# Optimization experiments

Hardware: AMD Instinct MI355X
Metric: run time of the kernel (lower is better)

## Reference

```python
import jax, jax.numpy as jnp
import numpy as np

K = 16

def _knn_idx(pts, k):
    # pts: [B, 3, N] -> idx [B, N, k] (self-inclusive nearest neighbors)
    inner = -2.0 * jnp.einsum('bdn,bdm->bnm', pts, pts)
    xx = jnp.sum(pts * pts, axis=1)  # [B, N]
    pd = -xx[:, :, None] - inner - xx[:, None, :]  # negative squared distance
    _, idx = jax.lax.top_k(pd, k)
    return idx

def _gather(feats, idx):
    # feats: [B, N, D], idx: [B, N, k] -> [B, N, k, D]
    return jax.vmap(lambda f, i: f[i])(feats, idx)

def _conv1x1(x, w, b):
    # x: [B, Cin, N], w: [Cout, Cin], b: [Cout]
    return jnp.einsum('oi,bin->bon', w, x) + b[None, :, None]

def _linear(x, w, b):
    # x: [B, N, Din], w: [Dout, Din]
    return jnp.einsum('bnd,od->bno', x, w) + b

def _local_cov(pts, idx):
    # pts: [B, 3, N] -> [B, 12, N]
    nb = _gather(jnp.swapaxes(pts, 1, 2), idx)  # [B, N, k, 3]
    outer = nb[:, :, 0, :, None] * nb[:, :, 1, None, :]  # [B, N, 3, 3]
    B, N = pts.shape[0], pts.shape[2]
    outer = jnp.swapaxes(outer.reshape(B, N, 9), 1, 2)  # [B, 9, N]
    return jnp.concatenate([pts, outer], axis=1)

def _local_maxpool(x, idx):
    # x: [B, D, N] -> [B, N, D]
    nb = _gather(jnp.swapaxes(x, 1, 2), idx)  # [B, N, k, D]
    return jnp.max(nb, axis=2)

def setup_inputs() -> dict:
    key = jax.random.key(0)
    ks = jax.random.split(key, 20)
    def w(k, shape):
        return jax.random.normal(k, shape, dtype=jnp.float32) * 0.05
    pts = jax.random.normal(ks[0], (8, 3, 4096), dtype=jnp.float32)
    return {
        'pts': pts,
        'm1w1': w(ks[1], (64, 12)), 'm1b1': w(ks[2], (64,)),
        'm1w2': w(ks[3], (64, 64)), 'm1b2': w(ks[4], (64,)),
        'm1w3': w(ks[5], (64, 64)), 'm1b3': w(ks[6], (64,)),
        'l1w': w(ks[7], (64, 64)), 'l1b': w(ks[8], (64,)),
        'c1w': w(ks[9], (128, 64)), 'c1b': w(ks[10], (128,)),
        'l2w': w(ks[11], (128, 128)), 'l2b': w(ks[12], (128,)),
        'c2w': w(ks[13], (1024, 128)), 'c2b': w(ks[14], (1024,)),
        'm2w1': w(ks[15], (512, 1024)), 'm2b1': w(ks[16], (512,)),
        'm2w2': w(ks[17], (512, 512)), 'm2b2': w(ks[18], (512,)),
    }

def reference(pts, m1w1, m1b1, m1w2, m1b2, m1w3, m1b3, l1w, l1b,
              c1w, c1b, l2w, l2b, c2w, c2b, m2w1, m2b1, m2w2, m2b2):
    idx = _knn_idx(pts, K)  # [B, N, k]
    x = _local_cov(pts, idx)  # [B, 12, N]
    # mlp1: three 1x1 convs with ReLU
    x = jax.nn.relu(_conv1x1(x, m1w1, m1b1))
    x = jax.nn.relu(_conv1x1(x, m1w2, m1b2))
    x = jax.nn.relu(_conv1x1(x, m1w3, m1b3))  # [B, 64, N]
    # graph layer
    x = _local_maxpool(x, idx)          # [B, N, 64]
    x = _linear(x, l1w, l1b)            # [B, N, 64]
    x = jnp.swapaxes(x, 1, 2)           # [B, 64, N]
    x = jax.nn.relu(_conv1x1(x, c1w, c1b))  # [B, 128, N]
    x = _local_maxpool(x, idx)          # [B, N, 128]
    x = _linear(x, l2w, l2b)            # [B, N, 128]
    x = jnp.swapaxes(x, 1, 2)           # [B, 128, N]
    x = _conv1x1(x, c2w, c2b)           # [B, 1024, N]
    # global max pool
    x = jnp.max(x, axis=2, keepdims=True)  # [B, 1024, 1]
    # mlp2
    x = jax.nn.relu(_conv1x1(x, m2w1, m2b1))
    x = _conv1x1(x, m2w2, m2b2)  # [B, 512, 1]
    return x.reshape(-1, 512)
```

## Files before the change

### kernel.cpp

```cpp
#include <hip/hip_runtime.h>
#include <cfloat>

#define NBATCH 8
#define NPTS   4096
#define KNN    16
#define PPB    32
#define NSL    8
#define CAP    24

__device__ __forceinline__ float relu_f(float x) { return x > 0.f ? x : 0.f; }

__global__ __launch_bounds__(256)
void knn_kernel(const float* __restrict__ pts, int* __restrict__ idxout)
{
    __shared__ __align__(16) float4 tile[NSL * 129];
    __shared__ float  kl[PPB * NSL * 8];
    __shared__ float  thr[PPB];
    __shared__ int    cnt[PPB];

    const int b = blockIdx.y, tid = threadIdx.x;
    const int ptl = tid >> 3, r = tid & 7;
    const int n = blockIdx.x * PPB + ptl;
    const float* pb = pts + (size_t)b * 3 * NPTS;

    const float sx = pb[n], sy = pb[NPTS + n], sz = pb[2 * NPTS + n];

    float k8[8];
#pragma unroll
    for (int s = 0; s < 8; ++s) k8[s] = -FLT_MAX;

    const float4* slice = tile + r * 129;

    for (int t = 0; t < 4; ++t) {
        if (t) __syncthreads();
        for (int i = tid; i < 1024; i += 256) {
            int j = t * 1024 + i;
            float x = pb[j], y = pb[NPTS + j], z = pb[2 * NPTS + j];
            float xx = __fadd_rn(__fadd_rn(__fmul_rn(x, x), __fmul_rn(y, y)),
                                 __fmul_rn(z, z));
            tile[(i >> 7) * 129 + (i & 127)] = make_float4(x, y, z, xx);
        }
        __syncthreads();
#pragma unroll 8
        for (int ii = 0; ii < 128; ++ii) {
            float4 c = slice[ii];
            float dt = __fmaf_rn(sx, c.x, __fmaf_rn(sy, c.y, __fmul_rn(sz, c.z)));
            float pd = __fmaf_rn(2.f, dt, -c.w);
            float old0 = k8[0];
#pragma unroll
            for (int s = 7; s >= 1; --s)
                k8[s] = __builtin_amdgcn_fmed3f(k8[s - 1], k8[s], pd);
            k8[0] = fmaxf(old0, pd);
        }
    }

#pragma unroll
    for (int s = 0; s < 8; ++s) kl[(ptl * NSL + r) * 8 + s] = k8[s];
    __syncthreads();

    if (r == 0) {
        const float* L = kl + ptl * 64;
        int p0 = 0, p1 = 0, p2 = 0, p3 = 0, p4 = 0, p5 = 0, p6 = 0, p7 = 0;
        float tv = 0.f;
        for (int o = 0; o < 16; ++o) {
            float v0 = (p0 < 8) ? L[p0]      : -FLT_MAX;
            float v1 = (p1 < 8) ? L[8 + p1]  : -FLT_MAX;
            float v2 = (p2 < 8) ? L[16 + p2] : -FLT_MAX;
            float v3 = (p3 < 8) ? L[24 + p3] : -FLT_MAX;
            float v4 = (p4 < 8) ? L[32 + p4] : -FLT_MAX;
            float v5 = (p5 < 8) ? L[40 + p5] : -FLT_MAX;
            float v6 = (p6 < 8) ? L[48 + p6] : -FLT_MAX;
            float v7 = (p7 < 8) ? L[56 + p7] : -FLT_MAX;
            float m = fmaxf(fmaxf(fmaxf(v0, v1), fmaxf(v2, v3)),
                            fmaxf(fmaxf(v4, v5), fmaxf(v6, v7)));
            tv = m;
            if      (v0 == m) ++p0;
            else if (v1 == m) ++p1;
            else if (v2 == m) ++p2;
            else if (v3 == m) ++p3;
            else if (v4 == m) ++p4;
            else if (v5 == m) ++p5;
            else if (v6 == m) ++p6;
            else              ++p7;
        }
        thr[ptl] = tv;
        cnt[ptl] = 0;
    }
    __syncthreads();
    const float myThr = thr[ptl];

    float* pv = kl;
    int*   pi = (int*)(kl + PPB * CAP);

    for (int tt = 0; tt < 4; ++tt) {
        int t = 3 - tt;
        if (tt) {
            __syncthreads();
            for (int i = tid; i < 1024; i += 256) {
                int j = t * 1024 + i;
                float x = pb[j], y = pb[NPTS + j], z = pb[2 * NPTS + j];
                float xx = __fadd_rn(__fadd_rn(__fmul_rn(x, x), __fmul_rn(y, y)),
                                     __fmul_rn(z, z));
                tile[(i >> 7) * 129 + (i & 127)] = make_float4(x, y, z, xx);
            }
            __syncthreads();
        }
#pragma unroll 8
        for (int ii = 0; ii < 128; ++ii) {
            float4 c = slice[ii];
            float dt = __fmaf_rn(sx, c.x, __fmaf_rn(sy, c.y, __fmul_rn(sz, c.z)));
            float pd = __fmaf_rn(2.f, dt, -c.w);
            if (pd >= myThr) {
                int pos = atomicAdd(&cnt[ptl], 1);
                if (pos < CAP) {
                    pv[ptl * CAP + pos] = pd;
                    pi[ptl * CAP + pos] = t * 1024 + r * 128 + ii;
                }
            }
        }
    }
    __syncthreads();

    if (tid < PPB) {
        const int np = blockIdx.x * PPB + tid;
        int* out = idxout + ((size_t)b * NPTS + np) * KNN;
        int c = cnt[tid];
        if (c <= CAP) {
            float* v  = pv + tid * CAP;
            int*   ix = pi + tid * CAP;
            for (int o = 0; o < 16; ++o) {
                int best = o;
                for (int q = o + 1; q < c; ++q) {
                    float vq = v[q], vb = v[best];
                    if (vq > vb || (vq == vb && ix[q] < ix[best])) best = q;
                }
                float tv = v[o]; v[o] = v[best]; v[best] = tv;
                int   ti = ix[o]; ix[o] = ix[best]; ix[best] = ti;
                out[o] = ix[o];
            }
        } else {
            float qx = pb[np], qy = pb[NPTS + np], qz = pb[2 * NPTS + np];
            float v16[16]; int i16[16];
#pragma unroll
            for (int s = 0; s < 16; ++s) { v16[s] = -FLT_MAX; i16[s] = 0; }
            for (int j = 0; j < NPTS; ++j) {
                float x = pb[j], y = pb[NPTS + j], z = pb[2 * NPTS + j];
                float xx = __fadd_rn(__fadd_rn(__fmul_rn(x, x), __fmul_rn(y, y)),
                                     __fmul_rn(z, z));
                float dt = __fmaf_rn(qx, x, __fmaf_rn(qy, y, __fmul_rn(qz, z)));
                float pd = __fmaf_rn(2.f, dt, -xx);
                if (pd > v16[15]) {
                    int s = 15;
                    while (s > 0 && pd > v16[s - 1]) {
                        v16[s] = v16[s - 1]; i16[s] = i16[s - 1]; --s;
                    }
                    v16[s] = pd; i16[s] = j;
                }
            }
            for (int o = 0; o < 16; ++o) out[o] = i16[o];
        }
    }
}

__global__ __launch_bounds__(256)
void cov_mlp1_kernel(const float* __restrict__ pts, const int* __restrict__ idx,
                     const float* __restrict__ w1, const float* __restrict__ b1,
                     const float* __restrict__ w2, const float* __restrict__ b2,
                     const float* __restrict__ w3, const float* __restrict__ b3,
                     float* __restrict__ h3out)
{
    __shared__ __align__(16) float cov[64 * 16];
    __shared__ __align__(16) float w1s[64 * 16];
    __shared__ __align__(16) float w2s[64 * 68];
    __shared__ __align__(16) float w3s[64 * 68];
    __shared__ __align__(16) float hA[64 * 68];
    __shared__ __align__(16) float hB[64 * 68];

    const int b = blockIdx.y, tid = threadIdx.x;
    const int n0 = blockIdx.x * 64;
    const int pq = tid >> 4, cq = tid & 15;

    for (int i = tid; i < 64 * 4; i += 256) {
        int p = i >> 2, k4 = i & 3;
        float4 v = make_float4(0.f, 0.f, 0.f, 0.f);
        if (k4 < 3) v = *(const float4*)(w1 + p * 12 + k4 * 4);
        ((float4*)(w1s + p * 16))[k4] = v;
    }
    for (int i = tid; i < 64 * 16; i += 256) {
        int p = i >> 4, k4 = i & 15;
        ((float4*)(w2s + p * 68))[k4] = ((const float4*)(w2 + p * 64))[k4];
        ((float4*)(w3s + p * 68))[k4] = ((const float4*)(w3 + p * 64))[k4];
    }
    if (tid < 64) {
        const int n = n0 + tid;
        const int* ip = idx + ((size_t)b * NPTS + n) * KNN;
        int j0 = ip[0], j1 = ip[1];
        const float* pb = pts + (size_t)b * 3 * NPTS;
        float px = pb[n],  py = pb[NPTS + n],  pz = pb[2 * NPTS + n];
        float ax = pb[j0], ay = pb[NPTS + j0], az = pb[2 * NPTS + j0];
        float bx = pb[j1], by = pb[NPTS + j1], bz = pb[2 * NPTS + j1];
        float* cv = cov + tid * 16;
        cv[0] = px; cv[1] = py; cv[2] = pz;
        cv[3] = ax * bx; cv[4]  = ax * by; cv[5]  = ax * bz;
        cv[6] = ay * bx; cv[7]  = ay * by; cv[8]  = ay * bz;
        cv[9] = az * bx; cv[10] = az * by; cv[11] = az * bz;
        cv[12] = 0.f; cv[13] = 0.f; cv[14] = 0.f; cv[15] = 0.f;
    }
    __syncthreads();

    {
        float acc[4][4];
#pragma unroll
        for (int i = 0; i < 4; ++i)
#pragma unroll
            for (int j = 0; j < 4; ++j) acc[i][j] = 0.f;
        const float4* X4 = (const float4*)cov;
        const float4* W4 = (const float4*)w1s;
#pragma unroll
        for (int k4 = 0; k4 < 4; ++k4) {
            float4 xa[4], wb[4];
#pragma unroll
            for (int i = 0; i < 4; ++i) xa[i] = X4[(pq * 4 + i) * 4 + k4];
#pragma unroll
            for (int j = 0; j < 4; ++j) wb[j] = W4[(cq + 16 * j) * 4 + k4];
#pragma unroll
            for (int i = 0; i < 4; ++i)
#pragma unroll
                for (int j = 0; j < 4; ++j)
                    acc[i][j] += xa[i].x * wb[j].x + xa[i].y * wb[j].y
                               + xa[i].z * wb[j].z + xa[i].w * wb[j].w;
        }
#pragma unroll
        for (int j = 0; j < 4; ++j) {
            int c = cq + 16 * j;
            float bias = b1[c];
#pragma unroll
            for (int i = 0; i < 4; ++i)
                hA[(pq * 4 + i) * 68 + c] = relu_f(acc[i][j] + bias);
        }
    }
    __syncthreads();

    {
        float acc[4][4];
#pragma unroll
        for (int i = 0; i < 4; ++i)
#pragma unroll
            for (int j = 0; j < 4; ++j) acc[i][j] = 0.f;
        const float4* X4 = (const float4*)hA;
        const float4* W4 = (const float4*)w2s;
        for (int k4 = 0; k4 < 16; ++k4) {
            float4 xa[4], wb[4];
#pragma unroll
            for (int i = 0; i < 4; ++i) xa[i] = X4[(pq * 4 + i) * 17 + k4];
#pragma unroll
            for (int j = 0; j < 4; ++j) wb[j] = W4[(cq + 16 * j) * 17 + k4];
#pragma unroll
            for (int i = 0; i < 4; ++i)
#pragma unroll
                for (int j = 0; j < 4; ++j)
                    acc[i][j] += xa[i].x * wb[j].x + xa[i].y * wb[j].y
                               + xa[i].z * wb[j].z + xa[i].w * wb[j].w;
        }
#pragma unroll
        for (int j = 0; j < 4; ++j) {
            int c = cq + 16 * j;
            float bias = b2[c];
#pragma unroll
            for (int i = 0; i < 4; ++i)
                hB[(pq * 4 + i) * 68 + c] = relu_f(acc[i][j] + bias);
        }
    }
    __syncthreads();

    {
        float acc[4][4];
#pragma unroll
        for (int i = 0; i < 4; ++i)
#pragma unroll
            for (int j = 0; j < 4; ++j) acc[i][j] = 0.f;
        const float4* X4 = (const float4*)hB;
        const float4* W4 = (const float4*)w3s;
        for (int k4 = 0; k4 < 16; ++k4) {
            float4 xa[4], wb[4];
#pragma unroll
            for (int i = 0; i < 4; ++i) xa[i] = X4[(pq * 4 + i) * 17 + k4];
#pragma unroll
            for (int j = 0; j < 4; ++j) wb[j] = W4[(cq + 16 * j) * 17 + k4];
#pragma unroll
            for (int i = 0; i < 4; ++i)
#pragma unroll
                for (int j = 0; j < 4; ++j)
                    acc[i][j] += xa[i].x * wb[j].x + xa[i].y * wb[j].y
                               + xa[i].z * wb[j].z + xa[i].w * wb[j].w;
        }
#pragma unroll
        for (int j = 0; j < 4; ++j) {
            int c = cq + 16 * j;
            float bias = b3[c];
#pragma unroll
            for (int i = 0; i < 4; ++i)
                h3out[((size_t)b * NPTS + n0 + pq * 4 + i) * 64 + c] =
                    relu_f(acc[i][j] + bias);
        }
    }
}

template <int DV4>
__global__ __launch_bounds__(256)
void maxpool4_kernel(const float4* __restrict__ f, const int* __restrict__ idx,
                     float4* __restrict__ out)
{
    constexpr int SH = (DV4 == 16) ? 4 : 5;
    int t = blockIdx.x * 256 + threadIdx.x;
    int d4 = t & (DV4 - 1);
    int n  = (t >> SH) & (NPTS - 1);
    int b  = t >> (SH + 12);
    const int* ip = idx + ((size_t)b * NPTS + n) * KNN;
    const float4* fb = f + (size_t)b * NPTS * DV4;
    float4 v = make_float4(-FLT_MAX, -FLT_MAX, -FLT_MAX, -FLT_MAX);
#pragma unroll
    for (int k = 0; k < KNN; ++k) {
        float4 c = fb[(size_t)ip[k] * DV4 + d4];
        v.x = fmaxf(v.x, c.x); v.y = fmaxf(v.y, c.y);
        v.z = fmaxf(v.z, c.z); v.w = fmaxf(v.w, c.w);
    }
    out[t] = v;
}

__global__ __launch_bounds__(256)
void lin_conv1_kernel(const float* __restrict__ xin,
                      const float* __restrict__ l1w, const float* __restrict__ l1b,
                      const float* __restrict__ c1w, const float* __restrict__ c1b,
                      float* __restrict__ yout)
{
    __shared__ __align__(16) float sx[64 * 68];
    __shared__ __align__(16) float wbuf[64 * 68];
    __shared__ __align__(16) float t1[64 * 68];
    const int b = blockIdx.y, tid = threadIdx.x;
    const int n0 = blockIdx.x * 64;
    const int pq = tid >> 4, cq = tid & 15;

    for (int i = tid; i < 64 * 16; i += 256) {
        int p = i >> 4, k4 = i & 15;
        ((float4*)(sx + p * 68))[k4] =
            ((const float4*)(xin + ((size_t)b * NPTS + n0 + p) * 64))[k4];
        ((float4*)(wbuf + p * 68))[k4] = ((const float4*)(l1w + p * 64))[k4];
    }
    __syncthreads();

    {
        float acc[4][4];
#pragma unroll
        for (int i = 0; i < 4; ++i)
#pragma unroll
            for (int j = 0; j < 4; ++j) acc[i][j] = 0.f;
        const float4* X4 = (const float4*)sx;
        const float4* W4 = (const float4*)wbuf;
        for (int k4 = 0; k4 < 16; ++k4) {
            float4 xa[4], wb[4];
#pragma unroll
            for (int i = 0; i < 4; ++i) xa[i] = X4[(pq * 4 + i) * 17 + k4];
#pragma unroll
            for (int j = 0; j < 4; ++j) wb[j] = W4[(cq + 16 * j) * 17 + k4];
#pragma unroll
            for (int i = 0; i < 4; ++i)
#pragma unroll
                for (int j = 0; j < 4; ++j)
                    acc[i][j] += xa[i].x * wb[j].x + xa[i].y * wb[j].y
                               + xa[i].z * wb[j].z + xa[i].w * wb[j].w;
        }
#pragma unroll
        for (int j = 0; j < 4; ++j) {
            int c = cq + 16 * j;
            float bias = l1b[c];
#pragma unroll
            for (int i = 0; i < 4; ++i)
                t1[(pq * 4 + i) * 68 + c] = acc[i][j] + bias;
        }
    }

    for (int g = 0; g < 2; ++g) {
        __syncthreads();
        for (int i = tid; i < 64 * 16; i += 256) {
            int p = i >> 4, k4 = i & 15;
            ((float4*)(wbuf + p * 68))[k4] =
                ((const float4*)(c1w + (size_t)(g * 64 + p) * 64))[k4];
        }
        __syncthreads();
        float acc[4][4];
#pragma unroll
        for (int i = 0; i < 4; ++i)
#pragma unroll
            for (int j = 0; j < 4; ++j) acc[i][j] = 0.f;
        const float4* X4 = (const float4*)t1;
        const float4* W4 = (const float4*)wbuf;
        for (int k4 = 0; k4 < 16; ++k4) {
            float4 xa[4], wb[4];
#pragma unroll
            for (int i = 0; i < 4; ++i) xa[i] = X4[(pq * 4 + i) * 17 + k4];
#pragma unroll
            for (int j = 0; j < 4; ++j) wb[j] = W4[(cq + 16 * j) * 17 + k4];
#pragma unroll
            for (int i = 0; i < 4; ++i)
#pragma unroll
                for (int j = 0; j < 4; ++j)
                    acc[i][j] += xa[i].x * wb[j].x + xa[i].y * wb[j].y
                               + xa[i].z * wb[j].z + xa[i].w * wb[j].w;
        }
#pragma unroll
        for (int j = 0; j < 4; ++j) {
            int c = g * 64 + cq + 16 * j;
            float bias = c1b[c];
#pragma unroll
            for (int i = 0; i < 4; ++i)
                yout[((size_t)b * NPTS + n0 + pq * 4 + i) * 128 + c] =
                    relu_f(acc[i][j] + bias);
        }
    }
}

__global__ __launch_bounds__(256)
void lin2_kernel(const float* __restrict__ xin, const float* __restrict__ w,
                 const float* __restrict__ bias, float* __restrict__ out)
{
    __shared__ __align__(16) float Xs[64 * 132];
    __shared__ __align__(16) float Ws[64 * 132];
    const int chunk = blockIdx.x, g = blockIdx.y, b = blockIdx.z;
    const int tid = threadIdx.x;

    for (int i = tid; i < 64 * 32; i += 256) {
        int p = i >> 5, k4 = i & 31;
        ((float4*)(Xs + p * 132))[k4] =
            ((const float4*)(xin + ((size_t)b * NPTS + chunk * 64 + p) * 128))[k4];
        ((float4*)(Ws + p * 132))[k4] =
            ((const float4*)(w + (size_t)(g * 64 + p) * 128))[k4];
    }
    __syncthreads();

    const int pq = tid >> 4, cq = tid & 15;
    const float4* X4 = (const float4*)Xs;
    const float4* W4 = (const float4*)Ws;
    float acc[4][4];
#pragma unroll
    for (int i = 0; i < 4; ++i)
#pragma unroll
        for (int j = 0; j < 4; ++j) acc[i][j] = 0.f;

    for (int k4 = 0; k4 < 32; ++k4) {
        float4 xa[4], wb[4];
#pragma unroll
        for (int i = 0; i < 4; ++i) xa[i] = X4[(pq * 4 + i) * 33 + k4];
#pragma unroll
        for (int j = 0; j < 4; ++j) wb[j] = W4[(cq + 16 * j) * 33 + k4];
#pragma unroll
        for (int i = 0; i < 4; ++i)
#pragma unroll
            for (int j = 0; j < 4; ++j)
                acc[i][j] += xa[i].x * wb[j].x + xa[i].y * wb[j].y
                           + xa[i].z * wb[j].z + xa[i].w * wb[j].w;
    }
#pragma unroll
    for (int j = 0; j < 4; ++j) {
        int c = g * 64 + cq + 16 * j;
        float bv = bias[c];
#pragma unroll
        for (int i = 0; i < 4; ++i)
            out[((size_t)b * NPTS + chunk * 64 + pq * 4 + i) * 128 + c] =
                acc[i][j] + bv;
    }
}

__global__ __launch_bounds__(256)
void conv2max_kernel(const float* __restrict__ xin, const float* __restrict__ w,
                     const float* __restrict__ bias, float* __restrict__ pmax)
{
    __shared__ __align__(16) float Xs[128 * 68];
    __shared__ __align__(16) float Ws[128 * 68];
    const int chunk = blockIdx.x, g = blockIdx.y, b = blockIdx.z;
    const int tid = threadIdx.x;
    const int pq = tid >> 4, cq = tid & 15;

    float acc[8][8];
#pragma unroll
    for (int i = 0; i < 8; ++i)
#pragma unroll
        for (int j = 0; j < 8; ++j) acc[i][j] = 0.f;

    for (int h = 0; h < 2; ++h) {
        __syncthreads();
        for (int i = tid; i < 128 * 16; i += 256) {
            int p = i >> 4, k4 = i & 15;
            ((float4*)(Xs + p * 68))[k4] = *(const float4*)
                (xin + ((size_t)b * NPTS + chunk * 128 + p) * 128 + h * 64 + k4 * 4);
            ((float4*)(Ws + p * 68))[k4] = *(const float4*)
                (w + (size_t)(g * 128 + p) * 128 + h * 64 + k4 * 4);
        }
        __syncthreads();

        const float4* X4 = (const float4*)Xs;
        const float4* W4 = (const float4*)Ws;

        float4 xA[8], wA[8], xB[8], wB[8];
#pragma unroll
        for (int i = 0; i < 8; ++i) {
            xA[i] = X4[(pq + 16 * i) * 17];
            wA[i] = W4[(cq + 16 * i) * 17];
        }
        for (int k4 = 0; k4 < 16; k4 += 2) {
#pragma unroll
            for (int i = 0; i < 8; ++i) {
                xB[i] = X4[(pq + 16 * i) * 17 + k4 + 1];
                wB[i] = W4[(cq + 16 * i) * 17 + k4 + 1];
            }
#pragma unroll
            for (int i = 0; i < 8; ++i)
#pragma unroll
                for (int j = 0; j < 8; ++j)
                    acc[i][j] += xA[i].x * wA[j].x + xA[i].y * wA[j].y
                               + xA[i].z * wA[j].z + xA[i].w * wA[j].w;
#pragma unroll
            for (int i = 0; i < 8; ++i) {
                xA[i] = X4[(pq + 16 * i) * 17 + k4 + 2];
                wA[i] = W4[(cq + 16 * i) * 17 + k4 + 2];
            }
#pragma unroll
            for (int i = 0; i < 8; ++i)
#pragma unroll
                for (int j = 0; j < 8; ++j)
                    acc[i][j] += xB[i].x * wB[j].x + xB[i].y * wB[j].y
                               + xB[i].z * wB[j].z + xB[i].w * wB[j].w;
        }
    }

    __syncthreads();
    float* smax = Xs;
#pragma unroll
    for (int j = 0; j < 8; ++j) {
        float m = acc[0][j];
#pragma unroll
        for (int i = 1; i < 8; ++i) m = fmaxf(m, acc[i][j]);
        smax[pq * 132 + cq + 16 * j] = m;
    }
    __syncthreads();
    if (tid < 128) {
        float v = smax[tid];
#pragma unroll
        for (int q = 1; q < 16; ++q) v = fmaxf(v, smax[q * 132 + tid]);
        int c = g * 128 + tid;
        pmax[((size_t)b * 32 + chunk) * 1024 + c] = v + bias[c];
    }
}

__global__ __launch_bounds__(256)
void gmax_kernel(const float* __restrict__ pmax, float* __restrict__ gmax)
{
    int t = blockIdx.x * 256 + threadIdx.x;
    int b = t >> 10, ch = t & 1023;
    const float* pp = pmax + (size_t)b * 32 * 1024 + ch;
    float v = -FLT_MAX;
    for (int c = 0; c < 32; ++c) v = fmaxf(v, pp[c * 1024]);
    gmax[t] = v;
}

__global__ __launch_bounds__(128)
void mlp2a_kernel(const float* __restrict__ g, const float* __restrict__ w1,
                  const float* __restrict__ b1, float* __restrict__ h)
{
    __shared__ __align__(16) float sg[1024];
    const int b = blockIdx.y, tid = threadIdx.x;
    for (int i = tid; i < 1024; i += 128) sg[i] = g[b * 1024 + i];
    __syncthreads();
    const int ch = blockIdx.x * 128 + tid;
    const float4* xr = (const float4*)sg;
    const float4* wr = (const float4*)(w1 + (size_t)ch * 1024);
    float a0 = 0.f, a1 = 0.f, a2 = 0.f, a3 = 0.f;
    for (int k = 0; k < 256; ++k) {
        float4 w = wr[k], x = xr[k];
        a0 += w.x * x.x; a1 += w.y * x.y; a2 += w.z * x.z; a3 += w.w * x.w;
    }
    h[b * 512 + ch] = relu_f(b1[ch] + ((a0 + a1) + (a2 + a3)));
}

__global__ __launch_bounds__(128)
void mlp2b_kernel(const float* __restrict__ h, const float* __restrict__ w2,
                  const float* __restrict__ b2, float* __restrict__ out)
{
    __shared__ __align__(16) float sh[512];
    const int b = blockIdx.y, tid = threadIdx.x;
    for (int i = tid; i < 512; i += 128) sh[i] = h[b * 512 + i];
    __syncthreads();
    const int ch = blockIdx.x * 128 + tid;
    const float4* xr = (const float4*)sh;
    const float4* wr = (const float4*)(w2 + (size_t)ch * 512);
    float a0 = 0.f, a1 = 0.f, a2 = 0.f, a3 = 0.f;
    for (int k = 0; k < 128; ++k) {
        float4 w = wr[k], x = xr[k];
        a0 += w.x * x.x; a1 += w.y * x.y; a2 += w.z * x.z; a3 += w.w * x.w;
    }
    out[b * 512 + ch] = b2[ch] + ((a0 + a1) + (a2 + a3));
}

extern "C" void kernel_launch(void* const* d_in, const int* in_sizes, int n_in,
                              void* d_out, int out_size, void* d_ws, size_t ws_size,
                              hipStream_t stream)
{
    const float* pts  = (const float*)d_in[0];
    const float* m1w1 = (const float*)d_in[1];
    const float* m1b1 = (const float*)d_in[2];
    const float* m1w2 = (const float*)d_in[3];
    const float* m1b2 = (const float*)d_in[4];
    const float* m1w3 = (const float*)d_in[5];
    const float* m1b3 = (const float*)d_in[6];
    const float* l1w  = (const float*)d_in[7];
    const float* l1b  = (const float*)d_in[8];
    const float* c1w  = (const float*)d_in[9];
    const float* c1b  = (const float*)d_in[10];
    const float* l2w  = (const float*)d_in[11];
    const float* l2b  = (const float*)d_in[12];
    const float* c2w  = (const float*)d_in[13];
    const float* c2b  = (const float*)d_in[14];
    const float* m2w1 = (const float*)d_in[15];
    const float* m2b1 = (const float*)d_in[16];
    const float* m2w2 = (const float*)d_in[17];
    const float* m2b2 = (const float*)d_in[18];

    char* ws = (char*)d_ws;
    size_t off = 0;
    int*   idx   = (int*)(ws + off);   off += (size_t)NBATCH * NPTS * KNN * 4;
    float* h3    = (float*)(ws + off); off += (size_t)NBATCH * NPTS * 64 * 4;
    float* mp1   = (float*)(ws + off); off += (size_t)NBATCH * NPTS * 64 * 4;
    float* y1    = (float*)(ws + off); off += (size_t)NBATCH * NPTS * 128 * 4;
    float* mp2   = (float*)(ws + off); off += (size_t)NBATCH * NPTS * 128 * 4;
    float* pmaxb = (float*)(ws + off); off += (size_t)NBATCH * 64 * 1024 * 4;
    float* gmx   = (float*)(ws + off); off += (size_t)NBATCH * 1024 * 4;
    float* hbuf  = (float*)(ws + off); off += (size_t)NBATCH * 512 * 4;
    float* t2    = y1;

    knn_kernel<<<dim3(NPTS / PPB, NBATCH), 256, 0, stream>>>(pts, idx);
    cov_mlp1_kernel<<<dim3(64, NBATCH), 256, 0, stream>>>(pts, idx, m1w1, m1b1,
                                                          m1w2, m1b2, m1w3, m1b3, h3);
    maxpool4_kernel<16><<<dim3(NBATCH * NPTS * 16 / 256), 256, 0, stream>>>(
        (const float4*)h3, idx, (float4*)mp1);
    lin_conv1_kernel<<<dim3(64, NBATCH), 256, 0, stream>>>(mp1, l1w, l1b, c1w, c1b, y1);
    maxpool4_kernel<32><<<dim3(NBATCH * NPTS * 32 / 256), 256, 0, stream>>>(
        (const float4*)y1, idx, (float4*)mp2);
    lin2_kernel<<<dim3(64, 2, NBATCH), 256, 0, stream>>>(mp2, l2w, l2b, t2);
    conv2max_kernel<<<dim3(32, 8, NBATCH), 256, 0, stream>>>(t2, c2w, c2b, pmaxb);
    gmax_kernel<<<dim3(32), 256, 0, stream>>>(pmaxb, gmx);
    mlp2a_kernel<<<dim3(4, NBATCH), 128, 0, stream>>>(gmx, m2w1, m2b1, hbuf);
    mlp2b_kernel<<<dim3(4, NBATCH), 128, 0, stream>>>(hbuf, m2w2, m2b2, (float*)d_out);
}
```

Before: 350.9 us.

## Run conv2 GEMM on bf16 MFMA with hi/lo split for fp32 accuracy

The 1024x128 conv2 GEMM with fused max-reduction now runs on bf16 MFMA instructions instead of scalar FP32 FMAs. To keep near-fp32 accuracy, activations and weights are split into bf16 high and low parts and three MFMA products are summed per tile. lin2 now emits the split activations directly, and a small extra kernel splits the weights on every call. The change trades extra MFMA work and a new launch for much higher matrix throughput, and accuracy is slightly lower than true fp32.

```diff
diff --git a/kernel.cpp b/kernel.cpp
--- a/kernel.cpp
+++ b/kernel.cpp
@@ -8,7 +8,22 @@
 #define NSL    8
 #define CAP    24
 
+typedef unsigned short u16;
+typedef __attribute__((ext_vector_type(8))) short short8;
+typedef __attribute__((ext_vector_type(4))) float f32x4;
+
 __device__ __forceinline__ float relu_f(float x) { return x > 0.f ? x : 0.f; }
+
+__device__ __forceinline__ void bf16_split(float v, u16& hi, u16& lo)
+{
+    unsigned u = __float_as_uint(v);
+    unsigned hb = (u + 0x7FFFu + ((u >> 16) & 1u)) >> 16;
+    float hf = __uint_as_float(hb << 16);
+    float l = v - hf;
+    unsigned ul = __float_as_uint(l);
+    unsigned lb = (ul + 0x7FFFu + ((ul >> 16) & 1u)) >> 16;
+    hi = (u16)hb; lo = (u16)lb;
+}
 
 __global__ __launch_bounds__(256)
 void knn_kernel(const float* __restrict__ pts, int* __restrict__ idxout)
@@ -422,7 +437,8 @@
 
 __global__ __launch_bounds__(256)
 void lin2_kernel(const float* __restrict__ xin, const float* __restrict__ w,
-                 const float* __restrict__ bias, float* __restrict__ out)
+                 const float* __restrict__ bias,
+                 u16* __restrict__ xhi, u16* __restrict__ xlo)
 {
     __shared__ __align__(16) float Xs[64 * 132];
     __shared__ __align__(16) float Ws[64 * 132];
@@ -465,88 +481,111 @@
         int c = g * 64 + cq + 16 * j;
         float bv = bias[c];
 #pragma unroll
-        for (int i = 0; i < 4; ++i)
-            out[((size_t)b * NPTS + chunk * 64 + pq * 4 + i) * 128 + c] =
-                acc[i][j] + bv;
-    }
-}
-
-__global__ __launch_bounds__(256)
-void conv2max_kernel(const float* __restrict__ xin, const float* __restrict__ w,
-                     const float* __restrict__ bias, float* __restrict__ pmax)
-{
-    __shared__ __align__(16) float Xs[128 * 68];
-    __shared__ __align__(16) float Ws[128 * 68];
+        for (int i = 0; i < 4; ++i) {
+            float v = acc[i][j] + bv;
+            size_t oidx = ((size_t)b * NPTS + chunk * 64 + pq * 4 + i) * 128 + c;
+            u16 h, l;
+            bf16_split(v, h, l);
+            xhi[oidx] = h; xlo[oidx] = l;
+        }
+    }
+}
+
+__global__ __launch_bounds__(256)
+void wsplit_kernel(const float* __restrict__ w, u16* __restrict__ whi,
+                   u16* __restrict__ wlo)
+{
+    int t = blockIdx.x * 256 + threadIdx.x;
+    u16 h, l;
+    bf16_split(w[t], h, l);
+    whi[t] = h; wlo[t] = l;
+}
+
+__global__ __launch_bounds__(256)
+void conv2max_mfma(const u16* __restrict__ xhi, const u16* __restrict__ xlo,
+                   const u16* __restrict__ whi, const u16* __restrict__ wlo,
+                   const float* __restrict__ bias, float* __restrict__ pmax)
+{
+    __shared__ __align__(16) u16 lds[4 * 16384];
+    u16* Wh = lds;
+    u16* Wl = lds + 16384;
+    u16* Xh = lds + 2 * 16384;
+    u16* Xl = lds + 3 * 16384;
+
     const int chunk = blockIdx.x, g = blockIdx.y, b = blockIdx.z;
     const int tid = threadIdx.x;
-    const int pq = tid >> 4, cq = tid & 15;
-
-    float acc[8][8];
-#pragma unroll
-    for (int i = 0; i < 8; ++i)
-#pragma unroll
-        for (int j = 0; j < 8; ++j) acc[i][j] = 0.f;
-
-    for (int h = 0; h < 2; ++h) {
-        __syncthreads();
-        for (int i = tid; i < 128 * 16; i += 256) {
-            int p = i >> 4, k4 = i & 15;
-            ((float4*)(Xs + p * 68))[k4] = *(const float4*)
-                (xin + ((size_t)b * NPTS + chunk * 128 + p) * 128 + h * 64 + k4 * 4);
-            ((float4*)(Ws + p * 68))[k4] = *(const float4*)
-                (w + (size_t)(g * 128 + p) * 128 + h * 64 + k4 * 4);
-        }
-        __syncthreads();
-
-        const float4* X4 = (const float4*)Xs;
-        const float4* W4 = (const float4*)Ws;
-
-        float4 xA[8], wA[8], xB[8], wB[8];
-#pragma unroll
-        for (int i = 0; i < 8; ++i) {
-            xA[i] = X4[(pq + 16 * i) * 17];
-            wA[i] = W4[(cq + 16 * i) * 17];
-        }
-        for (int k4 = 0; k4 < 16; k4 += 2) {
-#pragma unroll
-            for (int i = 0; i < 8; ++i) {
-                xB[i] = X4[(pq + 16 * i) * 17 + k4 + 1];
-                wB[i] = W4[(cq + 16 * i) * 17 + k4 + 1];
+    const int lane = tid & 63, wave = tid >> 6;
+    const int l15 = lane & 15, l4 = lane >> 4;
+    const int wm = wave >> 1, wn = wave & 1;
+
+    const u16* wh_g = whi + (size_t)g * 128 * 128;
+    const u16* wl_g = wlo + (size_t)g * 128 * 128;
+    const u16* xh_g = xhi + ((size_t)b * NPTS + chunk * 128) * 128;
+    const u16* xl_g = xlo + ((size_t)b * NPTS + chunk * 128) * 128;
+
+    for (int u = tid; u < 2048; u += 256) {
+        int row = u & 127, seg = u >> 7;
+        int lo_ = seg * 1024 + row * 8;
+        int go_ = row * 128 + seg * 8;
+        *(short8*)&Wh[lo_] = *(const short8*)&wh_g[go_];
+        *(short8*)&Wl[lo_] = *(const short8*)&wl_g[go_];
+        *(short8*)&Xh[lo_] = *(const short8*)&xh_g[go_];
+        *(short8*)&Xl[lo_] = *(const short8*)&xl_g[go_];
+    }
+    __syncthreads();
+
+    f32x4 acc[4][4];
+#pragma unroll
+    for (int mt = 0; mt < 4; ++mt)
+#pragma unroll
+        for (int nt = 0; nt < 4; ++nt)
+            acc[mt][nt] = (f32x4){0.f, 0.f, 0.f, 0.f};
+
+    for (int kb = 0; kb < 4; ++kb) {
+        const int seg = kb * 4 + l4;
+        short8 Ah[4], Al[4], Bh[4], Bl[4];
+#pragma unroll
+        for (int mt = 0; mt < 4; ++mt) {
+            int off = seg * 1024 + (wm * 64 + mt * 16 + l15) * 8;
+            Ah[mt] = *(const short8*)&Wh[off];
+            Al[mt] = *(const short8*)&Wl[off];
+        }
+#pragma unroll
+        for (int nt = 0; nt < 4; ++nt) {
+            int off = seg * 1024 + (wn * 64 + nt * 16 + l15) * 8;
+            Bh[nt] = *(const short8*)&Xh[off];
+            Bl[nt] = *(const short8*)&Xl[off];
+        }
+#pragma unroll
+        for (int mt = 0; mt < 4; ++mt)
+#pragma unroll
+            for (int nt = 0; nt < 4; ++nt) {
+                acc[mt][nt] = __builtin_amdgcn_mfma_f32_16x16x32_bf16(
+                    Ah[mt], Bh[nt], acc[mt][nt], 0, 0, 0);
+                acc[mt][nt] = __builtin_amdgcn_mfma_f32_16x16x32_bf16(
+                    Ah[mt], Bl[nt], acc[mt][nt], 0, 0, 0);
+                acc[mt][nt] = __builtin_amdgcn_mfma_f32_16x16x32_bf16(
+                    Al[mt], Bh[nt], acc[mt][nt], 0, 0, 0);
             }
-#pragma unroll
-            for (int i = 0; i < 8; ++i)
-#pragma unroll
-                for (int j = 0; j < 8; ++j)
-                    acc[i][j] += xA[i].x * wA[j].x + xA[i].y * wA[j].y
-                               + xA[i].z * wA[j].z + xA[i].w * wA[j].w;
-#pragma unroll
-            for (int i = 0; i < 8; ++i) {
-                xA[i] = X4[(pq + 16 * i) * 17 + k4 + 2];
-                wA[i] = W4[(cq + 16 * i) * 17 + k4 + 2];
-            }
-#pragma unroll
-            for (int i = 0; i < 8; ++i)
-#pragma unroll
-                for (int j = 0; j < 8; ++j)
-                    acc[i][j] += xB[i].x * wB[j].x + xB[i].y * wB[j].y
-                               + xB[i].z * wB[j].z + xB[i].w * wB[j].w;
-        }
-    }
-
-    __syncthreads();
-    float* smax = Xs;
-#pragma unroll
-    for (int j = 0; j < 8; ++j) {
-        float m = acc[0][j];
-#pragma unroll
-        for (int i = 1; i < 8; ++i) m = fmaxf(m, acc[i][j]);
-        smax[pq * 132 + cq + 16 * j] = m;
-    }
+    }
+
+    __syncthreads();
+    float* smax = (float*)lds;
+#pragma unroll
+    for (int mt = 0; mt < 4; ++mt)
+#pragma unroll
+        for (int r = 0; r < 4; ++r) {
+            float m = fmaxf(fmaxf(acc[mt][0][r], acc[mt][1][r]),
+                            fmaxf(acc[mt][2][r], acc[mt][3][r]));
+            int c = wm * 64 + mt * 16 + 4 * l4 + r;
+            smax[c * 33 + wn * 16 + l15] = m;
+        }
     __syncthreads();
     if (tid < 128) {
-        float v = smax[tid];
-#pragma unroll
-        for (int q = 1; q < 16; ++q) v = fmaxf(v, smax[q * 132 + tid]);
+        const float* row = smax + tid * 33;
+        float v = row[0];
+#pragma unroll
+        for (int j = 1; j < 32; ++j) v = fmaxf(v, row[j]);
         int c = g * 128 + tid;
         pmax[((size_t)b * 32 + chunk) * 1024 + c] = v + bias[c];
     }
@@ -635,8 +674,12 @@
     float* pmaxb = (float*)(ws + off); off += (size_t)NBATCH * 64 * 1024 * 4;
     float* gmx   = (float*)(ws + off); off += (size_t)NBATCH * 1024 * 4;
     float* hbuf  = (float*)(ws + off); off += (size_t)NBATCH * 512 * 4;
-    float* t2    = y1;
-
+    u16*   whi   = (u16*)(ws + off);   off += (size_t)1024 * 128 * 2;
+    u16*   wlo   = (u16*)(ws + off);   off += (size_t)1024 * 128 * 2;
+    u16*   xhi   = (u16*)y1;
+    u16*   xlo   = (u16*)((char*)y1 + (size_t)NBATCH * NPTS * 128 * 2);
+
+    wsplit_kernel<<<dim3(512), 256, 0, stream>>>(c2w, whi, wlo);
     knn_kernel<<<dim3(NPTS / PPB, NBATCH), 256, 0, stream>>>(pts, idx);
     cov_mlp1_kernel<<<dim3(64, NBATCH), 256, 0, stream>>>(pts, idx, m1w1, m1b1,
                                                           m1w2, m1b2, m1w3, m1b3, h3);
@@ -645,8 +688,9 @@
     lin_conv1_kernel<<<dim3(64, NBATCH), 256, 0, stream>>>(mp1, l1w, l1b, c1w, c1b, y1);
     maxpool4_kernel<32><<<dim3(NBATCH * NPTS * 32 / 256), 256, 0, stream>>>(
         (const float4*)y1, idx, (float4*)mp2);
-    lin2_kernel<<<dim3(64, 2, NBATCH), 256, 0, stream>>>(mp2, l2w, l2b, t2);
-    conv2max_kernel<<<dim3(32, 8, NBATCH), 256, 0, stream>>>(t2, c2w, c2b, pmaxb);
+    lin2_kernel<<<dim3(64, 2, NBATCH), 256, 0, stream>>>(mp2, l2w, l2b, xhi, xlo);
+    conv2max_mfma<<<dim3(32, 8, NBATCH), 256, 0, stream>>>(xhi, xlo, whi, wlo,
+                                                           c2b, pmaxb);
     gmax_kernel<<<dim3(32), 256, 0, stream>>>(pmaxb, gmx);
     mlp2a_kernel<<<dim3(4, NBATCH), 128, 0, stream>>>(gmx, m2w1, m2b1, hbuf);
     mlp2b_kernel<<<dim3(4, NBATCH), 128, 0, stream>>>(hbuf, m2w2, m2b2, (float*)d_out);
```

Result: faster. 319.1 us (-9.1%).
